# Kernel tuning notes

Measured on AMD Instinct MI355X. Metric: run time of the kernel, lower is better.

## Reference

```python
import jax, jax.numpy as jnp
import numpy as np

N = 50000
E = 800000
D = 128
NUM_GRAPHS = 64
NEG_SLOPE = 0.2


def _gat_conv(x, src, dst, W, a_src, a_dst, bias):
    """PyG GATConv with heads=1, concat=True. src/dst include self-loops."""
    h = x @ W                                  # [N, D_out]
    alpha_s = h @ a_src                        # [N]
    alpha_d = h @ a_dst                        # [N]
    e = alpha_s[src] + alpha_d[dst]            # [E_tot] edge scores
    e = jnp.where(e > 0, e, NEG_SLOPE * e)     # LeakyReLU(0.2)
    # numerically-stable softmax over incoming edges of each dst node
    m = jax.ops.segment_max(e, dst, num_segments=N)
    m = jnp.where(jnp.isfinite(m), m, 0.0)
    ex = jnp.exp(e - m[dst])
    s = jax.ops.segment_sum(ex, dst, num_segments=N)
    coef = ex / (s[dst] + 1e-16)               # [E_tot]
    msg = h[src] * coef[:, None]               # [E_tot, D_out] gathered messages
    out = jax.ops.segment_sum(msg, dst, num_segments=N)
    return out + bias


def setup_inputs() -> dict:
    key = jax.random.key(0)
    ks = jax.random.split(key, 12)
    x = jax.random.normal(ks[0], (N, D), dtype=jnp.float32)
    edge_index = jax.random.randint(ks[1], (2, E), 0, N, dtype=jnp.int64)
    batch = jnp.sort(jax.random.randint(ks[2], (N,), 0, NUM_GRAPHS, dtype=jnp.int64))
    g = 1.0 / np.sqrt(D)
    W1 = jax.random.normal(ks[3], (D, D), dtype=jnp.float32) * g
    as1 = jax.random.normal(ks[4], (D,), dtype=jnp.float32) * g
    ad1 = jax.random.normal(ks[5], (D,), dtype=jnp.float32) * g
    b1 = jnp.zeros((D,), dtype=jnp.float32)
    W2 = jax.random.normal(ks[6], (D, D), dtype=jnp.float32) * g
    as2 = jax.random.normal(ks[7], (D,), dtype=jnp.float32) * g
    ad2 = jax.random.normal(ks[8], (D,), dtype=jnp.float32) * g
    b2 = jnp.zeros((D,), dtype=jnp.float32)
    return {"x": x, "edge_index": edge_index, "batch": batch,
            "W1": W1, "as1": as1, "ad1": ad1, "b1": b1,
            "W2": W2, "as2": as2, "ad2": ad2, "b2": b2}


def reference(x, edge_index, batch, W1, as1, ad1, b1, W2, as2, ad2, b2):
    # PyG GATConv adds self-loops by default
    loops = jnp.arange(N, dtype=edge_index.dtype)
    src = jnp.concatenate([edge_index[0], loops])
    dst = jnp.concatenate([edge_index[1], loops])
    feats = _gat_conv(x, src, dst, W1, as1, ad1, b1)
    feats = _gat_conv(feats, src, dst, W2, as2, ad2, b2)
    # global mean pool over graphs in the batch
    sums = jax.ops.segment_sum(feats, batch, num_segments=NUM_GRAPHS)
    counts = jax.ops.segment_sum(jnp.ones((N,), feats.dtype), batch, num_segments=NUM_GRAPHS)
    pooled = sums / jnp.maximum(counts, 1.0)[:, None]
    return feats, pooled
```

## Files before the change

kernel.cpp:

```cpp
#include <hip/hip_runtime.h>

#define NN 50000
#define NE 800000
#define DIM 128
#define NG 64
#define ETOT (NE + NN)
#define NEG_SLOPE 0.2f
#define PB 200
#define MAXLG 8
#define NSH 8
#define SHW ((NN + NSH - 1) / NSH)
#define NB_SCAN ((NN + 255) / 256)
#define CAP 512

typedef unsigned int uint32;
typedef unsigned short ushort;
typedef short bf16x8 __attribute__((ext_vector_type(8)));
typedef float f32x4 __attribute__((ext_vector_type(4)));

static __device__ __forceinline__ uint32 f2bf_pack(float lo, float hi) {
  uint32 a = __float_as_uint(lo), b = __float_as_uint(hi);
  a = (a + 0x7fffu + ((a >> 16) & 1u)) >> 16;
  b = (b + 0x7fffu + ((b >> 16) & 1u)) >> 16;
  return a | (b << 16);
}
static __device__ __forceinline__ ushort f2bf1(float x) {
  uint32 a = __float_as_uint(x);
  a = (a + 0x7fffu + ((a >> 16) & 1u)) >> 16;
  return (ushort)a;
}
static __device__ __forceinline__ float bf_lo(uint32 u) { return __uint_as_float(u << 16); }
static __device__ __forceinline__ float bf_hi(uint32 u) { return __uint_as_float(u & 0xffff0000u); }


__global__ __launch_bounds__(256) void k_init(const float* __restrict__ W1, const float* __restrict__ W2,
                                              ushort* __restrict__ wt1, ushort* __restrict__ wt2,
                                              int* deg, int* fill, float* pooled, float* cnt) {
  int i = blockIdx.x * 256 + threadIdx.x;
  if (i < NN) { deg[i] = 1; fill[i] = 1; }
  if (i < NG * DIM) pooled[i] = 0.f;
  if (i < NG) cnt[i] = 0.f;
  if (i < DIM * DIM) {
    int n = i >> 7, k = i & 127;
    wt1[i] = f2bf1(W1[k * DIM + n]);
    wt2[i] = f2bf1(W2[k * DIM + n]);
  }
}

__global__ __launch_bounds__(256) void k_count(const int* __restrict__ dst, int* __restrict__ deg) {
  int e = blockIdx.x * 256 + threadIdx.x;
  if (e < NE) atomicAdd(&deg[dst[e]], 1);
}


__global__ __launch_bounds__(256) void k_scan1(const int* __restrict__ deg, int* __restrict__ offs,
                                               int* __restrict__ bsum) {
  __shared__ int ws[4];
  const int i = blockIdx.x * 256 + threadIdx.x;
  const int lane = threadIdx.x & 63, wid = threadIdx.x >> 6;
  int x = (i < NN) ? deg[i] : 0;
#pragma unroll
  for (int off = 1; off < 64; off <<= 1) {
    int t = __shfl_up(x, off, 64);
    if (lane >= off) x += t;
  }
  if (lane == 63) ws[wid] = x;
  __syncthreads();
  int pre = 0;
#pragma unroll
  for (int j = 0; j < 3; ++j) if (j < wid) pre += ws[j];
  x += pre;
  if (i < NN) offs[i + 1] = x;
  if (threadIdx.x == 255) bsum[blockIdx.x] = x;
}

__global__ __launch_bounds__(256) void k_scan2(const int* __restrict__ bsum, int* __restrict__ bpre) {
  __shared__ int ws[4];
  const int b = threadIdx.x;
  const int lane = b & 63, wid = b >> 6;
  int v = (b < NB_SCAN) ? bsum[b] : 0;
  int x = v;
#pragma unroll
  for (int off = 1; off < 64; off <<= 1) {
    int t = __shfl_up(x, off, 64);
    if (lane >= off) x += t;
  }
  if (lane == 63) ws[wid] = x;
  __syncthreads();
  int pre = 0;
#pragma unroll
  for (int j = 0; j < 3; ++j) if (j < wid) pre += ws[j];
  x += pre;
  if (b < NB_SCAN) bpre[b] = x - v;
}

__global__ __launch_bounds__(256) void k_scan3(int* __restrict__ offs, const int* __restrict__ bpre,
                                               const int* __restrict__ deg, int* __restrict__ csr) {
  const int i = blockIdx.x * 256 + threadIdx.x;
  if (i < NN) {
    int v = offs[i + 1] + bpre[blockIdx.x];
    offs[i + 1] = v;
    csr[v - deg[i]] = i;
  }
  if (i == 0) offs[0] = 0;
}

__global__ __launch_bounds__(256) void k_scatter(const int* __restrict__ src, const int* __restrict__ dst,
                                                 const int* __restrict__ offs, int* __restrict__ fill,
                                                 int* __restrict__ csr) {
  const int r = blockIdx.x & (NSH - 1);
  const int bi = blockIdx.x >> 3;
  const int nb = gridDim.x >> 3;
  const int lo = r * SHW, hi = min(lo + SHW, NN);
  for (int e = bi * 256 + threadIdx.x; e < NE; e += nb * 256) {
    int d = dst[e];
    if (d >= lo && d < hi) {
      int p = offs[d] + atomicAdd(&fill[d], 1);
      csr[p] = src[e];
    }
  }
}


template <int A16>
__global__ __launch_bounds__(256) void k_mm(const void* __restrict__ Xv, const ushort* __restrict__ WT,
                                            const float* __restrict__ a_s, const float* __restrict__ a_d,
                                            uint32* __restrict__ H16,
                                            float* __restrict__ alpha_s, float* __restrict__ alpha_d, int n) {
  __shared__ __align__(16) ushort sWT[DIM * DIM];
  __shared__ __align__(16) ushort sA[64 * DIM];
  const int tid = threadIdx.x;
  const int row0 = blockIdx.x * 64;

  {
    const int nr = tid >> 1, h2 = tid & 1;
    const uint4* wp = (const uint4*)(WT + nr * DIM + h2 * 64);
#pragma unroll
    for (int i = 0; i < 8; ++i) {
      uint4 v = wp[i];
      int byte = nr * 256 + (((h2 * 128 + i * 16)) ^ ((nr & 7) << 4));
      *(uint4*)((char*)sWT + byte) = v;
    }
  }
  {
    const int r = tid >> 2, q = tid & 3;
    int rg = row0 + r; if (rg > n - 1) rg = n - 1;
    if (A16) {
      const uint4* xp = (const uint4*)((const uint32*)Xv + (size_t)rg * 64 + q * 16);
#pragma unroll
      for (int i = 0; i < 4; ++i) {
        uint4 pk = xp[i];
        int byte = r * 256 + ((q * 64 + i * 16) ^ ((r & 7) << 4));
        *(uint4*)((char*)sA + byte) = pk;
      }
    } else {
      const float4* xp = (const float4*)((const float*)Xv + (size_t)rg * DIM + q * 32);
#pragma unroll
      for (int i = 0; i < 4; ++i) {
        float4 v0 = xp[2 * i], v1 = xp[2 * i + 1];
        uint4 pk = make_uint4(f2bf_pack(v0.x, v0.y), f2bf_pack(v0.z, v0.w),
                              f2bf_pack(v1.x, v1.y), f2bf_pack(v1.z, v1.w));
        int byte = r * 256 + ((q * 64 + i * 16) ^ ((r & 7) << 4));
        *(uint4*)((char*)sA + byte) = pk;
      }
    }
  }
  __syncthreads();

  const int l = tid & 63, wv = tid >> 6;
  const int jr = l & 15, g = l >> 4;
  const int m0 = wv * 16;
  f32x4 acc[8];
#pragma unroll
  for (int nt = 0; nt < 8; ++nt) acc[nt] = (f32x4){0.f, 0.f, 0.f, 0.f};

  const int ra = m0 + jr;
  const int abase = ra * 256, aswz = (ra & 7) << 4;
  const int bswz = (jr & 7) << 4;
#pragma unroll
  for (int kk = 0; kk < 4; ++kk) {
    const int kb = kk * 64 + g * 16;
    bf16x8 af = *(const bf16x8*)((const char*)sA + abase + (kb ^ aswz));
#pragma unroll
    for (int nt = 0; nt < 8; ++nt) {
      bf16x8 bfg = *(const bf16x8*)((const char*)sWT + (nt * 16 + jr) * 256 + (kb ^ bswz));
      acc[nt] = __builtin_amdgcn_mfma_f32_16x16x32_bf16(af, bfg, acc[nt], 0, 0, 0);
    }
  }

  float asv[8], adv[8];
#pragma unroll
  for (int nt = 0; nt < 8; ++nt) { asv[nt] = a_s[nt * 16 + jr]; adv[nt] = a_d[nt * 16 + jr]; }
#pragma unroll
  for (int j = 0; j < 4; ++j) {
    float ps = 0.f, pd = 0.f;
#pragma unroll
    for (int nt = 0; nt < 8; ++nt) {
      ps = fmaf(acc[nt][j], asv[nt], ps);
      pd = fmaf(acc[nt][j], adv[nt], pd);
    }
#pragma unroll
    for (int off = 1; off < 16; off <<= 1) {
      ps += __shfl_xor(ps, off, 64);
      pd += __shfl_xor(pd, off, 64);
    }
    int r = row0 + m0 + g * 4 + j;
    if (jr == 0 && r < n) { alpha_s[r] = ps; alpha_d[r] = pd; }
  }

  ushort* sOut = sA;
#pragma unroll
  for (int nt = 0; nt < 8; ++nt)
#pragma unroll
    for (int j = 0; j < 4; ++j)
      sOut[(m0 + g * 4 + j) * DIM + nt * 16 + jr] = f2bf1(acc[nt][j]);
#pragma unroll
  for (int i = 0; i < 4; ++i) {
    int r = row0 + m0 + (l >> 4) + i * 4;
    uint4 v = *(const uint4*)((const char*)sOut + m0 * 256 + l * 16 + i * 1024);
    if (r < n) *(uint4*)(H16 + (size_t)(row0 + m0) * 64 + l * 4 + i * 256) = v;
  }
}


template <int STORE16>
__global__ __launch_bounds__(256) void k_sma(const int* __restrict__ offs, const int* __restrict__ csr,
                                             const float* __restrict__ alpha_s, const float* __restrict__ alpha_d,
                                             const uint32* __restrict__ H16, const float* __restrict__ bias,
                                             float* __restrict__ out, uint32* __restrict__ out16) {
  __shared__ int2 s_pair[CAP];
  __shared__ int s_off[5];
  const int tid = threadIdx.x;
  const int n0 = blockIdx.x * 4;
  if (tid <= 4) s_off[tid] = offs[n0 + tid];
  __syncthreads();
  const int ebeg = s_off[0];
  const int nE = s_off[4] - ebeg;
  const int l = tid & 63, wv = tid >> 6;
  const int node = n0 + wv;
  const float2 bb = *(const float2*)(bias + 2 * l);
  float ax = 0.f, ay = 0.f, inv;

  if (nE <= CAP) {
    for (int e = tid; e < nE; e += 256) {
      int sv = csr[ebeg + e];
      s_pair[e] = make_int2(sv, __float_as_int(alpha_s[sv]));
    }
    __syncthreads();
    const int jb = s_off[wv] - ebeg, je = s_off[wv + 1] - ebeg;
    const float ad = alpha_d[node];
    float m = -1e30f;
    for (int j = jb + l; j < je; j += 64) {
      float sc = __int_as_float(s_pair[j].y) + ad;
      sc = sc > 0.f ? sc : NEG_SLOPE * sc;
      m = fmaxf(m, sc);
    }
#pragma unroll
    for (int off = 1; off < 64; off <<= 1) m = fmaxf(m, __shfl_xor(m, off, 64));
    float ssum = 0.f;
    for (int j = jb + l; j < je; j += 64) {
      float sc = __int_as_float(s_pair[j].y) + ad;
      sc = sc > 0.f ? sc : NEG_SLOPE * sc;
      float ex = __expf(sc - m);
      s_pair[j].y = __float_as_int(ex);
      ssum += ex;
    }
#pragma unroll
    for (int off = 1; off < 64; off <<= 1) ssum += __shfl_xor(ssum, off, 64);
    inv = 1.f / (ssum + 1e-16f);

    int j = jb;
    for (; j + 3 < je; j += 4) {
      int2 p0 = s_pair[j], p1 = s_pair[j + 1], p2 = s_pair[j + 2], p3 = s_pair[j + 3];
      uint32 v0 = H16[(size_t)p0.x * 64 + l];
      uint32 v1 = H16[(size_t)p1.x * 64 + l];
      uint32 v2 = H16[(size_t)p2.x * 64 + l];
      uint32 v3 = H16[(size_t)p3.x * 64 + l];
      float c0 = __int_as_float(p0.y), c1 = __int_as_float(p1.y);
      float c2 = __int_as_float(p2.y), c3 = __int_as_float(p3.y);
      ax = fmaf(c0, bf_lo(v0), ax); ay = fmaf(c0, bf_hi(v0), ay);
      ax = fmaf(c1, bf_lo(v1), ax); ay = fmaf(c1, bf_hi(v1), ay);
      ax = fmaf(c2, bf_lo(v2), ax); ay = fmaf(c2, bf_hi(v2), ay);
      ax = fmaf(c3, bf_lo(v3), ax); ay = fmaf(c3, bf_hi(v3), ay);
    }
    for (; j < je; ++j) {
      int2 p0 = s_pair[j];
      uint32 v0 = H16[(size_t)p0.x * 64 + l];
      float c0 = __int_as_float(p0.y);
      ax = fmaf(c0, bf_lo(v0), ax); ay = fmaf(c0, bf_hi(v0), ay);
    }
  } else {
    const int bg = offs[node], eg = offs[node + 1];
    const float ad = alpha_d[node];
    float m = -1e30f;
    for (int jj = bg + l; jj < eg; jj += 64) {
      float sc = alpha_s[csr[jj]] + ad;
      sc = sc > 0.f ? sc : NEG_SLOPE * sc;
      m = fmaxf(m, sc);
    }
#pragma unroll
    for (int off = 1; off < 64; off <<= 1) m = fmaxf(m, __shfl_xor(m, off, 64));
    float ssum = 0.f;
    for (int base = bg; base < eg; base += 64) {
      int cnt = min(64, eg - base);
      int sv = 0; float ex = 0.f;
      if (l < cnt) {
        sv = csr[base + l];
        float sc = alpha_s[sv] + ad;
        sc = sc > 0.f ? sc : NEG_SLOPE * sc;
        ex = __expf(sc - m);
      }
      ssum += ex;
      for (int jj = 0; jj < cnt; ++jj) {
        int s0 = __shfl(sv, jj, 64); float c0 = __shfl(ex, jj, 64);
        uint32 v0 = H16[(size_t)s0 * 64 + l];
        ax = fmaf(c0, bf_lo(v0), ax); ay = fmaf(c0, bf_hi(v0), ay);
      }
    }
#pragma unroll
    for (int off = 1; off < 64; off <<= 1) ssum += __shfl_xor(ssum, off, 64);
    inv = 1.f / (ssum + 1e-16f);
  }

  const float ox = ax * inv + bb.x, oy = ay * inv + bb.y;
  if (STORE16) out16[(size_t)node * 64 + l] = f2bf_pack(ox, oy);
  else *(float2*)(out + (size_t)node * DIM + 2 * l) = make_float2(ox, oy);
}


__global__ __launch_bounds__(256) void k_pool_partial(const float* __restrict__ feats,
                                                      const int* __restrict__ batch,
                                                      float* __restrict__ pooled, float* __restrict__ cnt) {
  __shared__ float acc[4][MAXLG][DIM];
  __shared__ float lcnt[4][MAXLG];
  const int tid = threadIdx.x;
  const int wid = tid >> 6, l = tid & 63;
  for (int i = tid; i < 4 * MAXLG * DIM; i += 256) ((float*)acc)[i] = 0.f;
  if (tid < 4 * MAXLG) ((float*)lcnt)[tid] = 0.f;
  __syncthreads();

  const int chunk = (NN + PB - 1) / PB;
  const int beg = blockIdx.x * chunk;
  const int end = min(beg + chunk, NN);
  const int g0 = (beg < NN) ? batch[beg] : 0;

  for (int node = beg + wid; node < end; node += 4) {
    int lg = batch[node] - g0;
    float2 v = *(const float2*)(feats + (size_t)node * DIM + 2 * l);
    if (lg < MAXLG) {
      acc[wid][lg][2 * l] += v.x;
      acc[wid][lg][2 * l + 1] += v.y;
      if (l == 0) lcnt[wid][lg] += 1.f;
    } else {
      atomicAdd(&pooled[(g0 + lg) * DIM + 2 * l], v.x);
      atomicAdd(&pooled[(g0 + lg) * DIM + 2 * l + 1], v.y);
      if (l == 0) atomicAdd(&cnt[g0 + lg], 1.f);
    }
  }
  __syncthreads();

  for (int i = tid; i < MAXLG * DIM; i += 256) {
    int lg = i >> 7, d = i & (DIM - 1);
    float s = acc[0][lg][d] + acc[1][lg][d] + acc[2][lg][d] + acc[3][lg][d];
    if (s != 0.f) atomicAdd(&pooled[(g0 + lg) * DIM + d], s);
  }
  if (tid < MAXLG) {
    float s = lcnt[0][tid] + lcnt[1][tid] + lcnt[2][tid] + lcnt[3][tid];
    if (s != 0.f) atomicAdd(&cnt[g0 + tid], s);
  }
}

__global__ __launch_bounds__(256) void k_pool_norm(float* pooled, const float* __restrict__ cnt) {
  int i = blockIdx.x * 256 + threadIdx.x;
  if (i < NG * DIM) pooled[i] /= fmaxf(cnt[i >> 7], 1.f);
}


static inline size_t pad256(size_t x) { return (x + 255) & ~(size_t)255; }

extern "C" void kernel_launch(void* const* d_in, const int* in_sizes, int n_in,
                              void* d_out, int out_size, void* d_ws, size_t ws_size,
                              hipStream_t stream) {
  const float* x   = (const float*)d_in[0];
  const int* ei    = (const int*)d_in[1];
  const int* batch = (const int*)d_in[2];
  const float* W1  = (const float*)d_in[3];
  const float* as1 = (const float*)d_in[4];
  const float* ad1 = (const float*)d_in[5];
  const float* b1  = (const float*)d_in[6];
  const float* W2  = (const float*)d_in[7];
  const float* as2 = (const float*)d_in[8];
  const float* ad2 = (const float*)d_in[9];
  const float* b2  = (const float*)d_in[10];

  float* out_feats = (float*)d_out;
  float* pooled    = out_feats + (size_t)NN * DIM;

  const int* src = ei;
  const int* dst = ei + NE;

  char* w = (char*)d_ws;
  uint32* h16 = (uint32*)w;   w += pad256((size_t)NN * 64 * 4);
  uint32* f116 = (uint32*)w;  w += pad256((size_t)NN * 64 * 4);
  float* alpha_s = (float*)w; w += pad256((size_t)NN * 4);
  float* alpha_d = (float*)w; w += pad256((size_t)NN * 4);
  int* deg  = (int*)w;        w += pad256((size_t)NN * 4);
  int* offs = (int*)w;        w += pad256((size_t)(NN + 1) * 4);
  int* fill = (int*)w;        w += pad256((size_t)NN * 4);
  int* csr  = (int*)w;        w += pad256((size_t)ETOT * 4);
  float* cnt  = (float*)w;    w += pad256((size_t)NG * 4);
  int* bsum = (int*)w;        w += pad256((size_t)NB_SCAN * 4);
  int* bpre = (int*)w;        w += pad256((size_t)NB_SCAN * 4);
  ushort* wt1 = (ushort*)w;   w += pad256((size_t)DIM * DIM * 2);
  ushort* wt2 = (ushort*)w;   w += pad256((size_t)DIM * DIM * 2);

  const int NB_N = (NN + 255) / 256;
  const int NB_E = (NE + 255) / 256;
  const int NB_A = NN / 4;
  const int NB_G = (NN + 63) / 64;
  const int NB_SC = 1024;

  k_init<<<NB_N, 256, 0, stream>>>(W1, W2, wt1, wt2, deg, fill, pooled, cnt);
  k_count<<<NB_E, 256, 0, stream>>>(dst, deg);
  k_scan1<<<NB_SCAN, 256, 0, stream>>>(deg, offs, bsum);
  k_scan2<<<1, 256, 0, stream>>>(bsum, bpre);
  k_scan3<<<NB_SCAN, 256, 0, stream>>>(offs, bpre, deg, csr);
  k_scatter<<<NB_SC, 256, 0, stream>>>(src, dst, offs, fill, csr);

  k_mm<0><<<NB_G, 256, 0, stream>>>(x, wt1, as1, ad1, h16, alpha_s, alpha_d, NN);
  k_sma<1><<<NB_A, 256, 0, stream>>>(offs, csr, alpha_s, alpha_d, h16, b1, nullptr, f116);

  k_mm<1><<<NB_G, 256, 0, stream>>>(f116, wt2, as2, ad2, h16, alpha_s, alpha_d, NN);
  k_sma<0><<<NB_A, 256, 0, stream>>>(offs, csr, alpha_s, alpha_d, h16, b2, out_feats, nullptr);

  k_pool_partial<<<PB, 256, 0, stream>>>(out_feats, batch, pooled, cnt);
  k_pool_norm<<<(NG * DIM + 255) / 256, 256, 0, stream>>>(pooled, cnt);
}
```

Before: 223.9 us.

## Split bf16 feature tables into column halves and aggregate per half-block

Stores the bf16 node feature matrices as two column-half arrays (64 columns each, 128 bytes per row) and launches twice as many aggregation blocks, each handling one half. Within a wave, the two 32-lane groups process alternating edges and are combined with a shuffle. The goal is to shrink each gathered table's footprint so it stays resident in cache during the random gathers, and to raise parallelism. The cost is that the softmax max/sum over each node's edges is computed twice, once per half-block, and each gather moves 128-byte rows instead of 256-byte rows.

Measured after the change: 261.0 us. +16.6%, slower.

```diff
diff --git a/kernel.cpp b/kernel.cpp
--- a/kernel.cpp
+++ b/kernel.cpp
@@ -123,9 +123,10 @@
 
 
 template <int A16>
-__global__ __launch_bounds__(256) void k_mm(const void* __restrict__ Xv, const ushort* __restrict__ WT,
+__global__ __launch_bounds__(256) void k_mm(const void* __restrict__ Xlo_v, const void* __restrict__ Xhi_v,
+                                            const ushort* __restrict__ WT,
                                             const float* __restrict__ a_s, const float* __restrict__ a_d,
-                                            uint32* __restrict__ H16,
+                                            uint32* __restrict__ Hlo, uint32* __restrict__ Hhi,
                                             float* __restrict__ alpha_s, float* __restrict__ alpha_d, int n) {
   __shared__ __align__(16) ushort sWT[DIM * DIM];
   __shared__ __align__(16) ushort sA[64 * DIM];
@@ -146,7 +147,8 @@
     const int r = tid >> 2, q = tid & 3;
     int rg = row0 + r; if (rg > n - 1) rg = n - 1;
     if (A16) {
-      const uint4* xp = (const uint4*)((const uint32*)Xv + (size_t)rg * 64 + q * 16);
+      const uint32* srcb = (q < 2) ? (const uint32*)Xlo_v : (const uint32*)Xhi_v;
+      const uint4* xp = (const uint4*)(srcb + (size_t)rg * 32 + (q & 1) * 16);
 #pragma unroll
       for (int i = 0; i < 4; ++i) {
         uint4 pk = xp[i];
@@ -154,7 +156,7 @@
         *(uint4*)((char*)sA + byte) = pk;
       }
     } else {
-      const float4* xp = (const float4*)((const float*)Xv + (size_t)rg * DIM + q * 32);
+      const float4* xp = (const float4*)((const float*)Xlo_v + (size_t)rg * DIM + q * 32);
 #pragma unroll
       for (int i = 0; i < 4; ++i) {
         float4 v0 = xp[2 * i], v1 = xp[2 * i + 1];
@@ -218,7 +220,11 @@
   for (int i = 0; i < 4; ++i) {
     int r = row0 + m0 + (l >> 4) + i * 4;
     uint4 v = *(const uint4*)((const char*)sOut + m0 * 256 + l * 16 + i * 1024);
-    if (r < n) *(uint4*)(H16 + (size_t)(row0 + m0) * 64 + l * 4 + i * 256) = v;
+    if (r < n) {
+      int c = (l & 15) * 4;
+      uint32* dstb = (c < 32) ? Hlo : Hhi;
+      *(uint4*)(dstb + (size_t)r * 32 + (c & 31)) = v;
+    }
   }
 }
 
@@ -226,19 +232,24 @@
 template <int STORE16>
 __global__ __launch_bounds__(256) void k_sma(const int* __restrict__ offs, const int* __restrict__ csr,
                                              const float* __restrict__ alpha_s, const float* __restrict__ alpha_d,
-                                             const uint32* __restrict__ H16, const float* __restrict__ bias,
-                                             float* __restrict__ out, uint32* __restrict__ out16) {
+                                             const uint32* __restrict__ Hlo, const uint32* __restrict__ Hhi,
+                                             const float* __restrict__ bias,
+                                             float* __restrict__ out,
+                                             uint32* __restrict__ f1lo, uint32* __restrict__ f1hi) {
   __shared__ int2 s_pair[CAP];
   __shared__ int s_off[5];
   const int tid = threadIdx.x;
-  const int n0 = blockIdx.x * 4;
+  const int half = blockIdx.x & 1;
+  const int n0 = (blockIdx.x >> 1) * 4;
   if (tid <= 4) s_off[tid] = offs[n0 + tid];
   __syncthreads();
   const int ebeg = s_off[0];
   const int nE = s_off[4] - ebeg;
   const int l = tid & 63, wv = tid >> 6;
+  const int sl = l & 31, g = l >> 5;
   const int node = n0 + wv;
-  const float2 bb = *(const float2*)(bias + 2 * l);
+  const uint32* __restrict__ Hh = half ? Hhi : Hlo;
+  const float2 bb = *(const float2*)(bias + half * 64 + 2 * sl);
   float ax = 0.f, ay = 0.f, inv;
 
   if (nE <= CAP) {
@@ -248,6 +259,7 @@
     }
     __syncthreads();
     const int jb = s_off[wv] - ebeg, je = s_off[wv + 1] - ebeg;
+    const int cnt = je - jb;
     const float ad = alpha_d[node];
     float m = -1e30f;
     for (int j = jb + l; j < je; j += 64) {
@@ -268,27 +280,26 @@
 #pragma unroll
     for (int off = 1; off < 64; off <<= 1) ssum += __shfl_xor(ssum, off, 64);
     inv = 1.f / (ssum + 1e-16f);
-
-    int j = jb;
-    for (; j + 3 < je; j += 4) {
-      int2 p0 = s_pair[j], p1 = s_pair[j + 1], p2 = s_pair[j + 2], p3 = s_pair[j + 3];
-      uint32 v0 = H16[(size_t)p0.x * 64 + l];
-      uint32 v1 = H16[(size_t)p1.x * 64 + l];
-      uint32 v2 = H16[(size_t)p2.x * 64 + l];
-      uint32 v3 = H16[(size_t)p3.x * 64 + l];
-      float c0 = __int_as_float(p0.y), c1 = __int_as_float(p1.y);
-      float c2 = __int_as_float(p2.y), c3 = __int_as_float(p3.y);
-      ax = fmaf(c0, bf_lo(v0), ax); ay = fmaf(c0, bf_hi(v0), ay);
-      ax = fmaf(c1, bf_lo(v1), ax); ay = fmaf(c1, bf_hi(v1), ay);
-      ax = fmaf(c2, bf_lo(v2), ax); ay = fmaf(c2, bf_hi(v2), ay);
-      ax = fmaf(c3, bf_lo(v3), ax); ay = fmaf(c3, bf_hi(v3), ay);
-    }
-    for (; j < je; ++j) {
-      int2 p0 = s_pair[j];
-      uint32 v0 = H16[(size_t)p0.x * 64 + l];
-      float c0 = __int_as_float(p0.y);
-      ax = fmaf(c0, bf_lo(v0), ax); ay = fmaf(c0, bf_hi(v0), ay);
-    }
+    int j = 0;
+    for (; j + 4 <= cnt; j += 4) {
+      int2 pA = s_pair[jb + j + g];
+      int2 pB = s_pair[jb + j + 2 + g];
+      uint32 vA = Hh[((uint32)pA.x << 5) + sl];
+      uint32 vB = Hh[((uint32)pB.x << 5) + sl];
+      float cA = __int_as_float(pA.y), cB = __int_as_float(pB.y);
+      ax = fmaf(cA, bf_lo(vA), ax); ay = fmaf(cA, bf_hi(vA), ay);
+      ax = fmaf(cB, bf_lo(vB), ax); ay = fmaf(cB, bf_hi(vB), ay);
+    }
+    for (; j < cnt; j += 2) {
+      int jj = j + g;
+      bool va = jj < cnt;
+      int2 p = s_pair[jb + (va ? jj : 0)];
+      float c = va ? __int_as_float(p.y) : 0.f;
+      uint32 v = Hh[((uint32)p.x << 5) + sl];
+      ax = fmaf(c, bf_lo(v), ax); ay = fmaf(c, bf_hi(v), ay);
+    }
+    ax += __shfl_xor(ax, 32, 64);
+    ay += __shfl_xor(ay, 32, 64);
   } else {
     const int bg = offs[node], eg = offs[node + 1];
     const float ad = alpha_d[node];
@@ -300,6 +311,7 @@
     }
 #pragma unroll
     for (int off = 1; off < 64; off <<= 1) m = fmaxf(m, __shfl_xor(m, off, 64));
+    const uint32* __restrict__ Hme = (l < 32) ? Hlo : Hhi;
     float ssum = 0.f;
     for (int base = bg; base < eg; base += 64) {
       int cnt = min(64, eg - base);
@@ -313,18 +325,27 @@
       ssum += ex;
       for (int jj = 0; jj < cnt; ++jj) {
         int s0 = __shfl(sv, jj, 64); float c0 = __shfl(ex, jj, 64);
-        uint32 v0 = H16[(size_t)s0 * 64 + l];
+        uint32 v0 = Hme[((uint32)s0 << 5) + sl];
         ax = fmaf(c0, bf_lo(v0), ax); ay = fmaf(c0, bf_hi(v0), ay);
       }
     }
 #pragma unroll
     for (int off = 1; off < 64; off <<= 1) ssum += __shfl_xor(ssum, off, 64);
     inv = 1.f / (ssum + 1e-16f);
-  }
-
-  const float ox = ax * inv + bb.x, oy = ay * inv + bb.y;
-  if (STORE16) out16[(size_t)node * 64 + l] = f2bf_pack(ox, oy);
-  else *(float2*)(out + (size_t)node * DIM + 2 * l) = make_float2(ox, oy);
+    float tx = __shfl(ax, half * 32 + sl, 64);
+    float ty = __shfl(ay, half * 32 + sl, 64);
+    ax = tx; ay = ty;
+  }
+
+  if (l < 32) {
+    const float ox = ax * inv + bb.x, oy = ay * inv + bb.y;
+    if (STORE16) {
+      uint32* f1h = half ? f1hi : f1lo;
+      f1h[(uint32)node * 32 + sl] = f2bf_pack(ox, oy);
+    } else {
+      *(float2*)(out + (size_t)node * DIM + half * 64 + 2 * sl) = make_float2(ox, oy);
+    }
+  }
 }
 
 
@@ -400,8 +421,10 @@
   const int* dst = ei + NE;
 
   char* w = (char*)d_ws;
-  uint32* h16 = (uint32*)w;   w += pad256((size_t)NN * 64 * 4);
-  uint32* f116 = (uint32*)w;  w += pad256((size_t)NN * 64 * 4);
+  uint32* hlo  = (uint32*)w;  w += pad256((size_t)NN * 32 * 4);
+  uint32* hhi  = (uint32*)w;  w += pad256((size_t)NN * 32 * 4);
+  uint32* f1lo = (uint32*)w;  w += pad256((size_t)NN * 32 * 4);
+  uint32* f1hi = (uint32*)w;  w += pad256((size_t)NN * 32 * 4);
   float* alpha_s = (float*)w; w += pad256((size_t)NN * 4);
   float* alpha_d = (float*)w; w += pad256((size_t)NN * 4);
   int* deg  = (int*)w;        w += pad256((size_t)NN * 4);
@@ -416,7 +439,7 @@
 
   const int NB_N = (NN + 255) / 256;
   const int NB_E = (NE + 255) / 256;
-  const int NB_A = NN / 4;
+  const int NB_A = (NN / 4) * 2;
   const int NB_G = (NN + 63) / 64;
   const int NB_SC = 1024;
 
@@ -427,11 +450,11 @@
   k_scan3<<<NB_SCAN, 256, 0, stream>>>(offs, bpre, deg, csr);
   k_scatter<<<NB_SC, 256, 0, stream>>>(src, dst, offs, fill, csr);
 
-  k_mm<0><<<NB_G, 256, 0, stream>>>(x, wt1, as1, ad1, h16, alpha_s, alpha_d, NN);
-  k_sma<1><<<NB_A, 256, 0, stream>>>(offs, csr, alpha_s, alpha_d, h16, b1, nullptr, f116);
-
-  k_mm<1><<<NB_G, 256, 0, stream>>>(f116, wt2, as2, ad2, h16, alpha_s, alpha_d, NN);
-  k_sma<0><<<NB_A, 256, 0, stream>>>(offs, csr, alpha_s, alpha_d, h16, b2, out_feats, nullptr);
+  k_mm<0><<<NB_G, 256, 0, stream>>>(x, nullptr, wt1, as1, ad1, hlo, hhi, alpha_s, alpha_d, NN);
+  k_sma<1><<<NB_A, 256, 0, stream>>>(offs, csr, alpha_s, alpha_d, hlo, hhi, b1, nullptr, f1lo, f1hi);
+
+  k_mm<1><<<NB_G, 256, 0, stream>>>(f1lo, f1hi, wt2, as2, ad2, hlo, hhi, alpha_s, alpha_d, NN);
+  k_sma<0><<<NB_A, 256, 0, stream>>>(offs, csr, alpha_s, alpha_d, hlo, hhi, b2, out_feats, nullptr, nullptr);
 
   k_pool_partial<<<PB, 256, 0, stream>>>(out_feats, batch, pooled, cnt);
   k_pool_norm<<<(NG * DIM + 255) / 256, 256, 0, stream>>>(pooled, cnt);
```
